# Performance work log

Hardware: AMD Instinct MI355X
Metric: run time of the kernel (lower is better)

Reference implementation:

```python
import jax, jax.numpy as jnp
import numpy as np

B, I, O, S, C = 64, 2048, 2048, 10, 512  # batch, input, output, dendritic segments, context dim


def setup_inputs() -> dict:
    key = jax.random.key(0)
    ks = jax.random.split(key, 8)
    x = jax.random.normal(ks[0], (B, I), dtype=jnp.float32)
    context = jax.random.normal(ks[1], (B, C), dtype=jnp.float32)
    prev_activation = jax.random.normal(ks[2], (B, I), dtype=jnp.float32)
    # sparse-initialized weight: randn/sqrt(I) * (rand > sparsity)
    w = jax.random.normal(ks[3], (O, I), dtype=jnp.float32) / np.sqrt(I)
    mask = (jax.random.uniform(ks[4], (O, I)) > 0.9).astype(jnp.float32)
    weight = w * mask
    bias = jnp.zeros((O,), dtype=jnp.float32)
    astrocyte_activation = jnp.ones((O,), dtype=jnp.float32)
    astrocyte_threshold = jnp.full((O,), 0.5, dtype=jnp.float32)
    dendrite_segments = jax.random.normal(ks[5], (O, I, S), dtype=jnp.float32) / np.sqrt(I)
    dendritic_gates = jnp.ones((O, S), dtype=jnp.float32)
    connection_strength = jnp.ones((O, I), dtype=jnp.float32)
    pruning_threshold = jnp.full((1,), 0.01, dtype=jnp.float32)
    return {
        "x": x, "context": context, "prev_activation": prev_activation,
        "weight": weight, "bias": bias,
        "astrocyte_activation": astrocyte_activation,
        "astrocyte_threshold": astrocyte_threshold,
        "dendrite_segments": dendrite_segments,
        "dendritic_gates": dendritic_gates,
        "connection_strength": connection_strength,
        "pruning_threshold": pruning_threshold,
    }


def reference(x, context, prev_activation, weight, bias, astrocyte_activation,
              astrocyte_threshold, dendrite_segments, dendritic_gates,
              connection_strength, pruning_threshold):
    dt = x.dtype
    # structural plasticity (eval branch): prune weak connections
    conn_mask = (jnp.abs(weight) * connection_strength > pruning_threshold[0]).astype(dt)
    eff_w = weight * conn_mask  # [O, I]
    # astrocyte modulation
    ctx_signal = jnp.mean(context, axis=-1, keepdims=True)          # [B, 1]
    astro = jax.nn.sigmoid(ctx_signal * astrocyte_activation[None, :])  # [B, O]
    astro = astro * (astro > astrocyte_threshold[None, :]).astype(dt)
    mean_astro = jnp.mean(astro, axis=0)                            # [O]
    mod_w = eff_w * mean_astro[:, None]                             # [O, I]
    synaptic = x @ mod_w.T + bias                                   # [B, O]
    # multi-compartment dendritic processing
    seg_act = jnp.einsum('bi,ois->bos', x, dendrite_segments)       # [B, O, S]
    gated = jax.nn.relu(seg_act) * jax.nn.sigmoid(dendritic_gates)[None, :, :]
    dendritic = jnp.sum(gated, axis=-1)                             # [B, O]
    return jax.nn.relu(synaptic + dendritic)
```

## Files before the change

### kernel.cpp

```cpp
#include <hip/hip_runtime.h>
#include <math.h>

#define Bn 64
#define In 2048
#define On 2048
#define Sn 10
#define Cn 512

#define OT 4
#define KT 64
#define NP 48
#define LROW 72
#define NSTAGE (In / KT)

typedef short short8 __attribute__((ext_vector_type(8)));
typedef float f32x4 __attribute__((ext_vector_type(4)));
typedef unsigned short ushort4v __attribute__((ext_vector_type(4)));

__device__ __forceinline__ unsigned short f2bf(float f) {
    union { float f; unsigned u; } v; v.f = f;
    unsigned r = (v.u + 0x7FFFu + ((v.u >> 16) & 1u)) >> 16;
    return (unsigned short)r;
}

__global__ void prep_kernel(const float* __restrict__ x,
                            const float* __restrict__ ctx,
                            float* __restrict__ ws_ctx,
                            unsigned short* __restrict__ ws_xbf) {
    const int b = blockIdx.x;
    const int t = threadIdx.x;
    if (b < Bn) {
        __shared__ float red[256];
        float s = ctx[b * Cn + t] + ctx[b * Cn + t + 256];
        red[t] = s;
        __syncthreads();
        for (int off = 128; off > 0; off >>= 1) {
            if (t < off) red[t] += red[t + off];
            __syncthreads();
        }
        if (t == 0) ws_ctx[b] = red[0] * (1.0f / (float)Cn);
    } else {
        int idx = (b - Bn) * 256 + t;
        ws_xbf[idx] = f2bf(x[idx]);
    }
}

__global__ __launch_bounds__(256, 2)
void main_kernel(const unsigned short* __restrict__ xbf,
                 const float* __restrict__ wgt,
                 const float* __restrict__ cst,
                 const float* __restrict__ seg,
                 const float* __restrict__ bias,
                 const float* __restrict__ aact,
                 const float* __restrict__ athr,
                 const float* __restrict__ gates,
                 const float* __restrict__ prn,
                 const float* __restrict__ ws_ctx,
                 float* __restrict__ out) {
    __shared__ __align__(16) unsigned short Alds[2][64 * LROW];
    __shared__ __align__(16) unsigned short Blds[2][NP * LROW];
    __shared__ float dsum[Bn][OT];
    __shared__ float ssum[Bn][OT];
    __shared__ float mastro[OT];

    const int t = threadIdx.x;
    const int o0 = blockIdx.x * OT;
    const int wave = t >> 6;
    const int lane = t & 63;
    const int l15 = lane & 15;
    const int q = lane >> 4;
    const float pthr = prn[0];

    ((float*)dsum)[t] = 0.0f;
    ((float*)ssum)[t] = 0.0f;

    for (int idx = t; idx < 4 * LROW; idx += 256) {
        Blds[0][44 * LROW + idx] = 0;
        Blds[1][44 * LROW + idx] = 0;
    }

    if (t < OT) {
        const int o = o0 + t;
        const float aa = aact[o], th = athr[o];
        float sum = 0.0f;
        for (int b2 = 0; b2 < Bn; ++b2) {
            float sg = 1.0f / (1.0f + expf(-ws_ctx[b2] * aa));
            if (sg > th) sum += sg;
        }
        mastro[t] = sum * (1.0f / (float)Bn);
    }

    const int s_o = t >> 6;
    const int s_i = t & 63;
    const float* segp = seg + ((size_t)(o0 + s_o) * In + s_i) * Sn;
    const int xm0 = t >> 3;
    const int xk0 = (t & 7) * 8;
    const int xm1 = 32 + (t >> 3);
    const int w_o = t >> 4;
    const int w_k = (t & 15) * 4;

    float sreg[10];
    short8 xv0, xv1;
    f32x4 wv, cv;

    auto load_stage = [&](int i0) {
        const float* sp = segp + (size_t)i0 * Sn;
#pragma unroll
        for (int r2 = 0; r2 < 5; ++r2) {
            float2 tmp = *(const float2*)(sp + r2 * 2);
            sreg[2 * r2] = tmp.x;
            sreg[2 * r2 + 1] = tmp.y;
        }
        xv0 = *(const short8*)(xbf + xm0 * In + i0 + xk0);
        xv1 = *(const short8*)(xbf + xm1 * In + i0 + xk0);
        if (t < 64) {
            wv = *(const f32x4*)(wgt + (size_t)(o0 + w_o) * In + i0 + w_k);
            cv = *(const f32x4*)(cst + (size_t)(o0 + w_o) * In + i0 + w_k);
        }
    };

    auto store_stage = [&](int bb) {
        unsigned short* Bp = &Blds[bb][(s_o * 10) * LROW + s_i];
#pragma unroll
        for (int s = 0; s < 10; ++s) Bp[s * LROW] = f2bf(sreg[s]);
        *(short8*)&Alds[bb][xm0 * LROW + xk0] = xv0;
        *(short8*)&Alds[bb][xm1 * LROW + xk0] = xv1;
        if (t < 64) {
            unsigned short ev[4];
#pragma unroll
            for (int j = 0; j < 4; ++j) {
                float wj = wv[j];
                float e = (__builtin_fabsf(wj) * cv[j] > pthr) ? wj : 0.0f;
                ev[j] = f2bf(e);
            }
            ushort4v e4 = {ev[0], ev[1], ev[2], ev[3]};
            *(ushort4v*)&Blds[bb][(40 + w_o) * LROW + w_k] = e4;
        }
    };

    f32x4 acc[3];
#pragma unroll
    for (int n = 0; n < 3; ++n) acc[n] = (f32x4){0.f, 0.f, 0.f, 0.f};

    auto compute = [&](int bb) {
        const unsigned short* Ap = &Alds[bb][(wave * 16 + l15) * LROW + q * 8];
        const unsigned short* Bp = &Blds[bb][l15 * LROW + q * 8];
#pragma unroll
        for (int ks = 0; ks < KT; ks += 32) {
            short8 a  = *(const short8*)(Ap + ks);
            short8 b0 = *(const short8*)(Bp + ks);
            short8 b1 = *(const short8*)(Bp + 16 * LROW + ks);
            short8 b2 = *(const short8*)(Bp + 32 * LROW + ks);
            acc[0] = __builtin_amdgcn_mfma_f32_16x16x32_bf16(a, b0, acc[0], 0, 0, 0);
            acc[1] = __builtin_amdgcn_mfma_f32_16x16x32_bf16(a, b1, acc[1], 0, 0, 0);
            acc[2] = __builtin_amdgcn_mfma_f32_16x16x32_bf16(a, b2, acc[2], 0, 0, 0);
        }
    };

    load_stage(0);
    store_stage(0);
    __syncthreads();
    int bb = 0;
    for (int it = 1; it < NSTAGE; ++it) {
        load_stage(it * KT);
        compute(bb);
        store_stage(bb ^ 1);
        __syncthreads();
        bb ^= 1;
    }
    compute(bb);

    const int brow = wave * 16 + q * 4;
#pragma unroll
    for (int nt = 0; nt < 3; ++nt) {
        const int n = nt * 16 + l15;
        if (n < 40) {
            const int ol = n / 10;
            const int s = n - ol * 10;
            const float g = 1.0f / (1.0f + expf(-gates[(o0 + ol) * Sn + s]));
#pragma unroll
            for (int r = 0; r < 4; ++r) {
                float v = acc[nt][r];
                v = v > 0.0f ? v : 0.0f;
                atomicAdd(&dsum[brow + r][ol], v * g);
            }
        } else if (n < 44) {
            const int ol = n - 40;
#pragma unroll
            for (int r = 0; r < 4; ++r) ssum[brow + r][ol] = acc[nt][r];
        }
    }
    __syncthreads();
    {
        const int m = t >> 2;
        const int ol = t & 3;
        const int o = o0 + ol;
        float v = dsum[m][ol] + mastro[ol] * ssum[m][ol] + bias[o];
        out[(size_t)m * On + o] = v > 0.0f ? v : 0.0f;
    }
}

extern "C" void kernel_launch(void* const* d_in, const int* in_sizes, int n_in,
                              void* d_out, int out_size, void* d_ws, size_t ws_size,
                              hipStream_t stream) {
    (void)in_sizes; (void)n_in; (void)out_size; (void)ws_size;
    const float* x    = (const float*)d_in[0];
    const float* ctx  = (const float*)d_in[1];
    const float* wgt  = (const float*)d_in[3];
    const float* bias = (const float*)d_in[4];
    const float* aact = (const float*)d_in[5];
    const float* athr = (const float*)d_in[6];
    const float* seg  = (const float*)d_in[7];
    const float* gat  = (const float*)d_in[8];
    const float* cst  = (const float*)d_in[9];
    const float* prn  = (const float*)d_in[10];
    float* out = (float*)d_out;

    float* ws_ctx = (float*)d_ws;
    unsigned short* ws_xbf = (unsigned short*)((char*)d_ws + 256);

    prep_kernel<<<Bn + (Bn * In) / 256, 256, 0, stream>>>(x, ctx, ws_ctx, ws_xbf);
    main_kernel<<<On / OT, 256, 0, stream>>>(ws_xbf, wgt, cst, seg, bias, aact,
                                             athr, gat, prn, ws_ctx, out);
}
```

Baseline: 291.0 us.

## Load x fragments directly into registers and deepen segment prefetch pipeline

Removes the shared-memory staging of the bf16 x tile: each wave now loads its MFMA A-operand fragments straight from global memory into registers. The segment, weight and connection-strength loads are remapped so consecutive threads read contiguous float2 chunks, and they are prefetched two stages ahead using ping-pong register sets while the loop is unrolled by two. This aims to cut LDS traffic and hide global-load latency of the dominant dendrite-segment stream. The cost is more registers and scalar bf16 stores into LDS, which may cause bank conflicts.

```diff
diff --git a/kernel.cpp b/kernel.cpp
--- a/kernel.cpp
+++ b/kernel.cpp
@@ -15,7 +15,6 @@
 
 typedef short short8 __attribute__((ext_vector_type(8)));
 typedef float f32x4 __attribute__((ext_vector_type(4)));
-typedef unsigned short ushort4v __attribute__((ext_vector_type(4)));
 
 __device__ __forceinline__ unsigned short f2bf(float f) {
     union { float f; unsigned u; } v; v.f = f;
@@ -57,7 +56,6 @@
                  const float* __restrict__ prn,
                  const float* __restrict__ ws_ctx,
                  float* __restrict__ out) {
-    __shared__ __align__(16) unsigned short Alds[2][64 * LROW];
     __shared__ __align__(16) unsigned short Blds[2][NP * LROW];
     __shared__ float dsum[Bn][OT];
     __shared__ float ssum[Bn][OT];
@@ -90,85 +88,94 @@
         mastro[t] = sum * (1.0f / (float)Bn);
     }
 
-    const int s_o = t >> 6;
-    const int s_i = t & 63;
-    const float* segp = seg + ((size_t)(o0 + s_o) * In + s_i) * Sn;
-    const int xm0 = t >> 3;
-    const int xk0 = (t & 7) * 8;
-    const int xm1 = 32 + (t >> 3);
-    const int w_o = t >> 4;
-    const int w_k = (t & 15) * 4;
-
-    float sreg[10];
-    short8 xv0, xv1;
-    f32x4 wv, cv;
-
-    auto load_stage = [&](int i0) {
-        const float* sp = segp + (size_t)i0 * Sn;
-#pragma unroll
-        for (int r2 = 0; r2 < 5; ++r2) {
-            float2 tmp = *(const float2*)(sp + r2 * 2);
-            sreg[2 * r2] = tmp.x;
-            sreg[2 * r2 + 1] = tmp.y;
-        }
-        xv0 = *(const short8*)(xbf + xm0 * In + i0 + xk0);
-        xv1 = *(const short8*)(xbf + xm1 * In + i0 + xk0);
-        if (t < 64) {
-            wv = *(const f32x4*)(wgt + (size_t)(o0 + w_o) * In + i0 + w_k);
-            cv = *(const f32x4*)(cst + (size_t)(o0 + w_o) * In + i0 + w_k);
-        }
-    };
-
-    auto store_stage = [&](int bb) {
-        unsigned short* Bp = &Blds[bb][(s_o * 10) * LROW + s_i];
-#pragma unroll
-        for (int s = 0; s < 10; ++s) Bp[s * LROW] = f2bf(sreg[s]);
-        *(short8*)&Alds[bb][xm0 * LROW + xk0] = xv0;
-        *(short8*)&Alds[bb][xm1 * LROW + xk0] = xv1;
-        if (t < 64) {
-            unsigned short ev[4];
-#pragma unroll
-            for (int j = 0; j < 4; ++j) {
-                float wj = wv[j];
-                float e = (__builtin_fabsf(wj) * cv[j] > pthr) ? wj : 0.0f;
-                ev[j] = f2bf(e);
-            }
-            ushort4v e4 = {ev[0], ev[1], ev[2], ev[3]};
-            *(ushort4v*)&Blds[bb][(40 + w_o) * LROW + w_k] = e4;
-        }
-    };
+    const float* segp[5];
+    int bofs[5];
+#pragma unroll
+    for (int j = 0; j < 5; ++j) {
+        const int f = t + 256 * j;
+        const int ol = f / 320;
+        const int rem = f - ol * 320;
+        const int io = rem / 5;
+        const int s2 = (rem - io * 5) * 2;
+        segp[j] = seg + ((size_t)(o0 + ol) * In + io) * Sn + s2;
+        bofs[j] = (ol * 10 + s2) * LROW + io;
+    }
+    const float* wptr = wgt + (size_t)(o0 + wave) * In + lane;
+    const float* cptr = cst + (size_t)(o0 + wave) * In + lane;
+    const int wofs = (40 + wave) * LROW + lane;
+    const unsigned short* aptr = xbf + (size_t)(wave * 16 + l15) * In + q * 8;
+
+    float2 svA[5], svB[5];
+    float wvA, cvA, wvB, cvB;
+    short8 aE0, aE1, aO0, aO1;
 
     f32x4 acc[3];
 #pragma unroll
     for (int n = 0; n < 3; ++n) acc[n] = (f32x4){0.f, 0.f, 0.f, 0.f};
 
-    auto compute = [&](int bb) {
-        const unsigned short* Ap = &Alds[bb][(wave * 16 + l15) * LROW + q * 8];
+    auto loadB = [&](float2 (&sv)[5], float& wv, float& cv, int i0) {
+        const int off = i0 * Sn;
+#pragma unroll
+        for (int j = 0; j < 5; ++j) sv[j] = *(const float2*)(segp[j] + off);
+        wv = wptr[i0];
+        cv = cptr[i0];
+    };
+    auto loadA = [&](short8& a0, short8& a1, int i0) {
+        a0 = *(const short8*)(aptr + i0);
+        a1 = *(const short8*)(aptr + i0 + 32);
+    };
+    auto storeB = [&](float2 (&sv)[5], float wv, float cv, int bb) {
+        unsigned short* Bl = Blds[bb];
+#pragma unroll
+        for (int j = 0; j < 5; ++j) {
+            Bl[bofs[j]] = f2bf(sv[j].x);
+            Bl[bofs[j] + LROW] = f2bf(sv[j].y);
+        }
+        const float e = (__builtin_fabsf(wv) * cv > pthr) ? wv : 0.0f;
+        Bl[wofs] = f2bf(e);
+    };
+    auto compute = [&](short8 a0, short8 a1, int bb) {
         const unsigned short* Bp = &Blds[bb][l15 * LROW + q * 8];
-#pragma unroll
-        for (int ks = 0; ks < KT; ks += 32) {
-            short8 a  = *(const short8*)(Ap + ks);
-            short8 b0 = *(const short8*)(Bp + ks);
-            short8 b1 = *(const short8*)(Bp + 16 * LROW + ks);
-            short8 b2 = *(const short8*)(Bp + 32 * LROW + ks);
-            acc[0] = __builtin_amdgcn_mfma_f32_16x16x32_bf16(a, b0, acc[0], 0, 0, 0);
-            acc[1] = __builtin_amdgcn_mfma_f32_16x16x32_bf16(a, b1, acc[1], 0, 0, 0);
-            acc[2] = __builtin_amdgcn_mfma_f32_16x16x32_bf16(a, b2, acc[2], 0, 0, 0);
-        }
-    };
-
-    load_stage(0);
-    store_stage(0);
+        short8 b0 = *(const short8*)(Bp);
+        short8 b1 = *(const short8*)(Bp + 16 * LROW);
+        short8 b2 = *(const short8*)(Bp + 32 * LROW);
+        acc[0] = __builtin_amdgcn_mfma_f32_16x16x32_bf16(a0, b0, acc[0], 0, 0, 0);
+        acc[1] = __builtin_amdgcn_mfma_f32_16x16x32_bf16(a0, b1, acc[1], 0, 0, 0);
+        acc[2] = __builtin_amdgcn_mfma_f32_16x16x32_bf16(a0, b2, acc[2], 0, 0, 0);
+        short8 c0 = *(const short8*)(Bp + 32);
+        short8 c1 = *(const short8*)(Bp + 16 * LROW + 32);
+        short8 c2 = *(const short8*)(Bp + 32 * LROW + 32);
+        acc[0] = __builtin_amdgcn_mfma_f32_16x16x32_bf16(a1, c0, acc[0], 0, 0, 0);
+        acc[1] = __builtin_amdgcn_mfma_f32_16x16x32_bf16(a1, c1, acc[1], 0, 0, 0);
+        acc[2] = __builtin_amdgcn_mfma_f32_16x16x32_bf16(a1, c2, acc[2], 0, 0, 0);
+    };
+
+    loadB(svA, wvA, cvA, 0);
+    loadB(svB, wvB, cvB, KT);
+    loadA(aE0, aE1, 0);
+    loadA(aO0, aO1, KT);
+    storeB(svA, wvA, cvA, 0);
+    loadB(svA, wvA, cvA, 2 * KT);
     __syncthreads();
-    int bb = 0;
-    for (int it = 1; it < NSTAGE; ++it) {
-        load_stage(it * KT);
-        compute(bb);
-        store_stage(bb ^ 1);
+
+    const int ILAST = (NSTAGE - 1) * KT;
+    for (int p = 0; p < NSTAGE / 2; ++p) {
+        const int itE = 2 * p;
+        const int itO = 2 * p + 1;
+        const int iE2 = (itE + 2 < NSTAGE) ? (itE + 2) * KT : ILAST;
+        const int iO2 = (itO + 2 < NSTAGE) ? (itO + 2) * KT : ILAST;
+        const int iA4 = (itE + 4 < NSTAGE) ? (itE + 4) * KT : ILAST;
+        compute(aE0, aE1, 0);
+        loadA(aE0, aE1, iE2);
+        storeB(svB, wvB, cvB, 1);
+        loadB(svB, wvB, cvB, iO2);
         __syncthreads();
-        bb ^= 1;
-    }
-    compute(bb);
+        compute(aO0, aO1, 1);
+        loadA(aO0, aO1, iO2);
+        storeB(svA, wvA, cvA, 0);
+        loadB(svA, wvA, cvA, iA4);
+        __syncthreads();
+    }
 
     const int brow = wave * 16 + q * 4;
 #pragma unroll
```

Measured after the change: 288.0 us. About the same (-1.1%).

## Restructure main kernel to one wave per output neuron with register-pipelined loads

Applied to the files above, without the earlier changes.

Changes the decomposition from 4 outputs per 256-thread block to one output per 64-thread single-wave block, giving 2048 blocks instead of 512. Each wave computes all 64 batch rows through 4 MFMA M-tiles and reads x fragments directly from global memory into registers instead of staging them in LDS. Segment, weight and connection loads are double-buffered in registers two stages ahead, so no block-wide barriers are needed. The epilogue replaces shared-memory atomics with wave shuffles. The cost is that every block rereads the full bf16 x matrix from global memory/L2, and the B tile is padded from 11 to 16 rows, wasting MFMA work.

```diff
diff --git a/kernel.cpp b/kernel.cpp
--- a/kernel.cpp
+++ b/kernel.cpp
@@ -7,21 +7,20 @@
 #define Sn 10
 #define Cn 512
 
-#define OT 4
 #define KT 64
-#define NP 48
+#define NT (In / KT)
 #define LROW 72
-#define NSTAGE (In / KT)
+#define NR 16
 
 typedef short short8 __attribute__((ext_vector_type(8)));
 typedef float f32x4 __attribute__((ext_vector_type(4)));
-typedef unsigned short ushort4v __attribute__((ext_vector_type(4)));
 
 __device__ __forceinline__ unsigned short f2bf(float f) {
     union { float f; unsigned u; } v; v.f = f;
     unsigned r = (v.u + 0x7FFFu + ((v.u >> 16) & 1u)) >> 16;
     return (unsigned short)r;
 }
+__device__ __forceinline__ float sigmoidf_(float x) { return 1.0f / (1.0f + expf(-x)); }
 
 __global__ void prep_kernel(const float* __restrict__ x,
                             const float* __restrict__ ctx,
@@ -45,7 +44,7 @@
     }
 }
 
-__global__ __launch_bounds__(256, 2)
+__global__ __launch_bounds__(64, 2)
 void main_kernel(const unsigned short* __restrict__ xbf,
                  const float* __restrict__ wgt,
                  const float* __restrict__ cst,
@@ -57,146 +56,125 @@
                  const float* __restrict__ prn,
                  const float* __restrict__ ws_ctx,
                  float* __restrict__ out) {
-    __shared__ __align__(16) unsigned short Alds[2][64 * LROW];
-    __shared__ __align__(16) unsigned short Blds[2][NP * LROW];
-    __shared__ float dsum[Bn][OT];
-    __shared__ float ssum[Bn][OT];
-    __shared__ float mastro[OT];
-
-    const int t = threadIdx.x;
-    const int o0 = blockIdx.x * OT;
-    const int wave = t >> 6;
-    const int lane = t & 63;
+    __shared__ __align__(16) unsigned short Blds[2][NR * LROW];
+
+    const int lane = threadIdx.x;
+    const int o = blockIdx.x;
     const int l15 = lane & 15;
     const int q = lane >> 4;
     const float pthr = prn[0];
 
-    ((float*)dsum)[t] = 0.0f;
-    ((float*)ssum)[t] = 0.0f;
-
-    for (int idx = t; idx < 4 * LROW; idx += 256) {
-        Blds[0][44 * LROW + idx] = 0;
-        Blds[1][44 * LROW + idx] = 0;
-    }
-
-    if (t < OT) {
-        const int o = o0 + t;
-        const float aa = aact[o], th = athr[o];
-        float sum = 0.0f;
-        for (int b2 = 0; b2 < Bn; ++b2) {
-            float sg = 1.0f / (1.0f + expf(-ws_ctx[b2] * aa));
-            if (sg > th) sum += sg;
-        }
-        mastro[t] = sum * (1.0f / (float)Bn);
-    }
-
-    const int s_o = t >> 6;
-    const int s_i = t & 63;
-    const float* segp = seg + ((size_t)(o0 + s_o) * In + s_i) * Sn;
-    const int xm0 = t >> 3;
-    const int xk0 = (t & 7) * 8;
-    const int xm1 = 32 + (t >> 3);
-    const int w_o = t >> 4;
-    const int w_k = (t & 15) * 4;
-
-    float sreg[10];
-    short8 xv0, xv1;
-    f32x4 wv, cv;
-
-    auto load_stage = [&](int i0) {
-        const float* sp = segp + (size_t)i0 * Sn;
-#pragma unroll
-        for (int r2 = 0; r2 < 5; ++r2) {
-            float2 tmp = *(const float2*)(sp + r2 * 2);
-            sreg[2 * r2] = tmp.x;
-            sreg[2 * r2 + 1] = tmp.y;
-        }
-        xv0 = *(const short8*)(xbf + xm0 * In + i0 + xk0);
-        xv1 = *(const short8*)(xbf + xm1 * In + i0 + xk0);
-        if (t < 64) {
-            wv = *(const f32x4*)(wgt + (size_t)(o0 + w_o) * In + i0 + w_k);
-            cv = *(const f32x4*)(cst + (size_t)(o0 + w_o) * In + i0 + w_k);
-        }
-    };
-
-    auto store_stage = [&](int bb) {
-        unsigned short* Bp = &Blds[bb][(s_o * 10) * LROW + s_i];
-#pragma unroll
-        for (int s = 0; s < 10; ++s) Bp[s * LROW] = f2bf(sreg[s]);
-        *(short8*)&Alds[bb][xm0 * LROW + xk0] = xv0;
-        *(short8*)&Alds[bb][xm1 * LROW + xk0] = xv1;
-        if (t < 64) {
-            unsigned short ev[4];
-#pragma unroll
-            for (int j = 0; j < 4; ++j) {
-                float wj = wv[j];
-                float e = (__builtin_fabsf(wj) * cv[j] > pthr) ? wj : 0.0f;
-                ev[j] = f2bf(e);
+    for (int idx = lane; idx < 5 * LROW; idx += 64) {
+        Blds[0][11 * LROW + idx] = 0;
+        Blds[1][11 * LROW + idx] = 0;
+    }
+
+    const float aa = aact[o], th = athr[o];
+    float sg = sigmoidf_(ws_ctx[lane] * aa);
+    float ma = (sg > th) ? sg : 0.0f;
+#pragma unroll
+    for (int m = 32; m; m >>= 1) ma += __shfl_xor(ma, m, 64);
+    const float mastro = ma * (1.0f / (float)Bn);
+
+    const float gsig = (l15 < 10) ? sigmoidf_(gates[o * Sn + l15]) : 0.0f;
+
+    int sego[5], ldso[5];
+#pragma unroll
+    for (int j = 0; j < 5; ++j) {
+        const int f = lane + 64 * j;
+        const int io = f / 5;
+        const int s2 = (f - io * 5) * 2;
+        sego[j] = io * Sn + s2;
+        ldso[j] = s2 * LROW + io;
+    }
+    const float* segbase = seg + (size_t)o * In * Sn;
+    const float* wrow = wgt + (size_t)o * In;
+    const float* crow = cst + (size_t)o * In;
+    const unsigned short* xrow = xbf + (size_t)l15 * In + q * 8;
+
+    float2 SA[5], SB[5];
+    float wA, cA, wB, cB;
+    short8 AA[4][2], AB[4][2];
+
+    f32x4 acc[4];
+#pragma unroll
+    for (int mt = 0; mt < 4; ++mt) acc[mt] = (f32x4){0.f, 0.f, 0.f, 0.f};
+
+    auto loadSeg = [&](float2 (&S)[5], float& w, float& c, int t) {
+        const float* p = segbase + t * (KT * Sn);
+#pragma unroll
+        for (int j = 0; j < 5; ++j) S[j] = *(const float2*)(p + sego[j]);
+        w = wrow[t * KT + lane];
+        c = crow[t * KT + lane];
+    };
+    auto loadA = [&](short8 (&A)[4][2], int t) {
+#pragma unroll
+        for (int mt = 0; mt < 4; ++mt) {
+            const unsigned short* p = xrow + (size_t)mt * 16 * In + t * KT;
+            A[mt][0] = *(const short8*)(p);
+            A[mt][1] = *(const short8*)(p + 32);
+        }
+    };
+    auto storeT = [&](float2 (&S)[5], float w, float c, int bb) {
+        unsigned short* B = Blds[bb];
+#pragma unroll
+        for (int j = 0; j < 5; ++j) {
+            B[ldso[j]] = f2bf(S[j].x);
+            B[ldso[j] + LROW] = f2bf(S[j].y);
+        }
+        const float e = (__builtin_fabsf(w) * c > pthr) ? w : 0.0f;
+        B[10 * LROW + lane] = f2bf(e);
+    };
+    auto computeT = [&](short8 (&A)[4][2], int bb) {
+        const unsigned short* Bp = &Blds[bb][l15 * LROW + q * 8];
+        short8 b0 = *(const short8*)(Bp);
+        short8 b1 = *(const short8*)(Bp + 32);
+#pragma unroll
+        for (int mt = 0; mt < 4; ++mt) {
+            acc[mt] = __builtin_amdgcn_mfma_f32_16x16x32_bf16(A[mt][0], b0, acc[mt], 0, 0, 0);
+            acc[mt] = __builtin_amdgcn_mfma_f32_16x16x32_bf16(A[mt][1], b1, acc[mt], 0, 0, 0);
+        }
+    };
+
+    loadSeg(SA, wA, cA, 0);
+    loadSeg(SB, wB, cB, 1);
+    loadA(AA, 0);
+    storeT(SA, wA, cA, 0);
+    for (int u = 0; u < NT / 2; ++u) {
+        const int t = 2 * u;
+        const int tp1 = (t + 1 < NT) ? t + 1 : NT - 1;
+        const int tp2 = (t + 2 < NT) ? t + 2 : NT - 1;
+        const int tp3 = (t + 3 < NT) ? t + 3 : NT - 1;
+        loadSeg(SA, wA, cA, tp2);
+        loadA(AB, tp1);
+        computeT(AA, 0);
+        storeT(SB, wB, cB, 1);
+        loadSeg(SB, wB, cB, tp3);
+        loadA(AA, tp2);
+        computeT(AB, 1);
+        storeT(SA, wA, cA, 0);
+    }
+
+    const float bo = bias[o];
+#pragma unroll
+    for (int mt = 0; mt < 4; ++mt) {
+#pragma unroll
+        for (int r = 0; r < 4; ++r) {
+            const float v = acc[mt][r];
+            float contrib;
+            if (l15 < 10)       contrib = (v > 0.f ? v : 0.f) * gsig;
+            else if (l15 == 10) contrib = mastro * v;
+            else                contrib = 0.f;
+            contrib += __shfl_xor(contrib, 1, 64);
+            contrib += __shfl_xor(contrib, 2, 64);
+            contrib += __shfl_xor(contrib, 4, 64);
+            contrib += __shfl_xor(contrib, 8, 64);
+            if (l15 == 0) {
+                const int b = mt * 16 + q * 4 + r;
+                const float ov = contrib + bo;
+                out[(size_t)b * On + o] = ov > 0.f ? ov : 0.f;
             }
-            ushort4v e4 = {ev[0], ev[1], ev[2], ev[3]};
-            *(ushort4v*)&Blds[bb][(40 + w_o) * LROW + w_k] = e4;
-        }
-    };
-
-    f32x4 acc[3];
-#pragma unroll
-    for (int n = 0; n < 3; ++n) acc[n] = (f32x4){0.f, 0.f, 0.f, 0.f};
-
-    auto compute = [&](int bb) {
-        const unsigned short* Ap = &Alds[bb][(wave * 16 + l15) * LROW + q * 8];
-        const unsigned short* Bp = &Blds[bb][l15 * LROW + q * 8];
-#pragma unroll
-        for (int ks = 0; ks < KT; ks += 32) {
-            short8 a  = *(const short8*)(Ap + ks);
-            short8 b0 = *(const short8*)(Bp + ks);
-            short8 b1 = *(const short8*)(Bp + 16 * LROW + ks);
-            short8 b2 = *(const short8*)(Bp + 32 * LROW + ks);
-            acc[0] = __builtin_amdgcn_mfma_f32_16x16x32_bf16(a, b0, acc[0], 0, 0, 0);
-            acc[1] = __builtin_amdgcn_mfma_f32_16x16x32_bf16(a, b1, acc[1], 0, 0, 0);
-            acc[2] = __builtin_amdgcn_mfma_f32_16x16x32_bf16(a, b2, acc[2], 0, 0, 0);
-        }
-    };
-
-    load_stage(0);
-    store_stage(0);
-    __syncthreads();
-    int bb = 0;
-    for (int it = 1; it < NSTAGE; ++it) {
-        load_stage(it * KT);
-        compute(bb);
-        store_stage(bb ^ 1);
-        __syncthreads();
-        bb ^= 1;
-    }
-    compute(bb);
-
-    const int brow = wave * 16 + q * 4;
-#pragma unroll
-    for (int nt = 0; nt < 3; ++nt) {
-        const int n = nt * 16 + l15;
-        if (n < 40) {
-            const int ol = n / 10;
-            const int s = n - ol * 10;
-            const float g = 1.0f / (1.0f + expf(-gates[(o0 + ol) * Sn + s]));
-#pragma unroll
-            for (int r = 0; r < 4; ++r) {
-                float v = acc[nt][r];
-                v = v > 0.0f ? v : 0.0f;
-                atomicAdd(&dsum[brow + r][ol], v * g);
-            }
-        } else if (n < 44) {
-            const int ol = n - 40;
-#pragma unroll
-            for (int r = 0; r < 4; ++r) ssum[brow + r][ol] = acc[nt][r];
-        }
-    }
-    __syncthreads();
-    {
-        const int m = t >> 2;
-        const int ol = t & 3;
-        const int o = o0 + ol;
-        float v = dsum[m][ol] + mastro[ol] * ssum[m][ol] + bias[o];
-        out[(size_t)m * On + o] = v > 0.0f ? v : 0.0f;
+        }
     }
 }
 
@@ -220,6 +198,6 @@
     unsigned short* ws_xbf = (unsigned short*)((char*)d_ws + 256);
 
     prep_kernel<<<Bn + (Bn * In) / 256, 256, 0, stream>>>(x, ctx, ws_ctx, ws_xbf);
-    main_kernel<<<On / OT, 256, 0, stream>>>(ws_xbf, wgt, cst, seg, bias, aact,
-                                             athr, gat, prn, ws_ctx, out);
-}
+    main_kernel<<<On, 64, 0, stream>>>(ws_xbf, wgt, cst, seg, bias, aact,
+                                       athr, gat, prn, ws_ctx, out);
+}
```

After: 298.5 us. 1.03x slower.
